# Performance work log

Measured on AMD Instinct MI355X. Metric: run time of the kernel, lower is better.

## Reference

```python
import jax, jax.numpy as jnp
import numpy as np

N_NODES = 100000
N_EDGES = 3200000
D_IN = 128
D_OUT = 128


def setup_inputs() -> dict:
    key = jax.random.key(0)
    k1, k2, k3, k4, k5, k6 = jax.random.split(key, 6)
    inputs = jax.random.normal(k1, (N_NODES, D_IN), dtype=jnp.float32)
    edge_row = jax.random.randint(k2, (N_EDGES,), 0, N_NODES, dtype=jnp.int32)
    edge_col = jax.random.randint(k3, (N_EDGES,), 0, N_NODES, dtype=jnp.int32)
    edge_weight = jax.random.uniform(k4, (N_EDGES,), dtype=jnp.float32)
    # xavier_uniform for [D_IN, D_OUT]
    limit = float(np.sqrt(6.0 / (D_IN + D_OUT)))
    weight = jax.random.uniform(k5, (D_IN, D_OUT), minval=-limit, maxval=limit, dtype=jnp.float32)
    bias = jnp.zeros((D_OUT,), dtype=jnp.float32)
    return {"inputs": inputs, "edge_row": edge_row, "edge_col": edge_col,
            "edge_weight": edge_weight, "weight": weight, "bias": bias}


def reference(inputs, edge_row, edge_col, edge_weight, weight, bias):
    # support = X @ W  -> [N, D_OUT]
    support = inputs @ weight
    # SpMM: out[i] = sum_{e: row[e]==i} w[e] * support[col[e]]
    messages = edge_weight[:, None] * support[edge_col]  # [E, D_OUT]
    out = jax.ops.segment_sum(messages, edge_row, num_segments=N_NODES)
    return out + bias
```

## Files before the change

kernel.cpp:

```cpp
#include <hip/hip_runtime.h>
#include <hip/hip_bf16.h>

#define D 128
#define BROWS 128
#define BSHIFT 7
#define BIN_CHUNK 16384
#define BCAP 5888
#define SORT_CAP 5120

typedef __attribute__((ext_vector_type(8))) short short8;
typedef __attribute__((ext_vector_type(4))) float f32x4;

static __device__ inline unsigned short f2bf(float x) {
    unsigned int u = __float_as_uint(x);
    return (unsigned short)((u + 0x7FFFu + ((u >> 16) & 1u)) >> 16);
}
static __device__ inline float bf2f(unsigned int h16) {
    return __uint_as_float(h16 << 16);
}

__global__ __launch_bounds__(256) void gemm_mfma_kernel(const float* __restrict__ X,
                                                        const float* __restrict__ W,
                                                        unsigned short* __restrict__ Sb,
                                                        int n_rows) {
    __shared__ unsigned char smem[49152];

    const int tid  = threadIdx.x;
    const int row0 = blockIdx.x * 64;

    #pragma unroll
    for (int i = 0; i < 8; ++i) {
        int idx = tid + i * 256;
        int r = idx >> 5, c4 = idx & 31;
        float4 v = make_float4(0.f, 0.f, 0.f, 0.f);
        if (row0 + r < n_rows) v = ((const float4*)(X + (size_t)(row0 + r) * D))[c4];
        uint2 pk;
        pk.x = (unsigned)f2bf(v.x) | ((unsigned)f2bf(v.y) << 16);
        pk.y = (unsigned)f2bf(v.z) | ((unsigned)f2bf(v.w) << 16);
        *(uint2*)(smem + r * 256 + ((c4 * 8) ^ ((r & 7) << 4))) = pk;
    }
    #pragma unroll
    for (int i = 0; i < 8; ++i) {
        int id = tid + i * 256;
        int n = id & 127, kc = id >> 7;
        float f0 = W[(size_t)(kc * 8 + 0) * D + n];
        float f1 = W[(size_t)(kc * 8 + 1) * D + n];
        float f2 = W[(size_t)(kc * 8 + 2) * D + n];
        float f3 = W[(size_t)(kc * 8 + 3) * D + n];
        float f4 = W[(size_t)(kc * 8 + 4) * D + n];
        float f5 = W[(size_t)(kc * 8 + 5) * D + n];
        float f6 = W[(size_t)(kc * 8 + 6) * D + n];
        float f7 = W[(size_t)(kc * 8 + 7) * D + n];
        unsigned pk0 = (unsigned)f2bf(f0) | ((unsigned)f2bf(f1) << 16);
        unsigned pk1 = (unsigned)f2bf(f2) | ((unsigned)f2bf(f3) << 16);
        unsigned pk2 = (unsigned)f2bf(f4) | ((unsigned)f2bf(f5) << 16);
        unsigned pk3 = (unsigned)f2bf(f6) | ((unsigned)f2bf(f7) << 16);
        *(uint4*)(smem + 16384 + n * 256 + ((kc * 16) ^ ((n & 7) << 4))) =
            make_uint4(pk0, pk1, pk2, pk3);
    }
    __syncthreads();

    const int wv  = __builtin_amdgcn_readfirstlane(tid >> 6);
    const int l15 = tid & 15;
    const int lhi = (tid & 63) >> 4;

    f32x4 acc[4][2];
    #pragma unroll
    for (int m = 0; m < 4; ++m)
        #pragma unroll
        for (int j = 0; j < 2; ++j) acc[m][j] = (f32x4){0.f, 0.f, 0.f, 0.f};

    #pragma unroll
    for (int ks = 0; ks < 4; ++ks) {
        const int kb = ks * 64 + lhi * 16;
        short8 a[4], b[2];
        #pragma unroll
        for (int m = 0; m < 4; ++m) {
            int r = m * 16 + l15;
            a[m] = *(const short8*)(smem + r * 256 + (kb ^ ((r & 7) << 4)));
        }
        #pragma unroll
        for (int j = 0; j < 2; ++j) {
            int n = wv * 32 + j * 16 + l15;
            b[j] = *(const short8*)(smem + 16384 + n * 256 + (kb ^ ((n & 7) << 4)));
        }
        #pragma unroll
        for (int m = 0; m < 4; ++m)
            #pragma unroll
            for (int j = 0; j < 2; ++j)
                acc[m][j] = __builtin_amdgcn_mfma_f32_16x16x32_bf16(a[m], b[j],
                                                                   acc[m][j], 0, 0, 0);
    }
    __syncthreads();

    #pragma unroll
    for (int m = 0; m < 4; ++m)
        #pragma unroll
        for (int j = 0; j < 2; ++j)
            #pragma unroll
            for (int r = 0; r < 4; ++r) {
                int row = m * 16 + lhi * 4 + r;
                int col = wv * 32 + j * 16 + l15;
                *(unsigned short*)(smem + row * 256 + ((col * 2) ^ ((row & 7) << 4))) =
                    f2bf(acc[m][j][r]);
            }
    __syncthreads();
    #pragma unroll
    for (int i = 0; i < 4; ++i) {
        int idx = tid + i * 256;
        int r = idx >> 4, kb = (idx & 15) * 16;
        uint4 v = *(const uint4*)(smem + r * 256 + (kb ^ ((r & 7) << 4)));
        int row = row0 + r;
        if (row < n_rows)
            *(uint4*)((unsigned char*)Sb + (size_t)row * 256 + kb) = v;
    }
}

__global__ __launch_bounds__(1024) void binit_kernel(int* __restrict__ curm, int nb) {
    int b = threadIdx.x;
    if (b < nb) curm[b] = b * BCAP;
}

__global__ __launch_bounds__(512) void bin_kernel(const int* __restrict__ erow,
                                                  const int* __restrict__ ecol,
                                                  const float* __restrict__ ew,
                                                  int* __restrict__ curm,
                                                  int2* __restrict__ binned,
                                                  int n_edges, int nb) {
    __shared__ int h[1024];
    __shared__ int base[1024];
    const int c0  = blockIdx.x * BIN_CHUNK;
    const int tid = threadIdx.x;
    int rows[BIN_CHUNK / 512];

    for (int i = tid; i < nb; i += 512) h[i] = 0;
    __syncthreads();
    #pragma unroll
    for (int k = 0; k < BIN_CHUNK / 512; ++k) {
        int e = c0 + k * 512 + tid;
        int r = (e < n_edges) ? erow[e] : -1;
        rows[k] = r;
        if (r >= 0) atomicAdd(&h[r >> BSHIFT], 1);
    }
    __syncthreads();
    for (int b = tid; b < nb; b += 512) {
        int c = h[b];
        if (c) base[b] = atomicAdd(&curm[b], c);
        h[b] = 0;
    }
    __syncthreads();
    #pragma unroll
    for (int k = 0; k < BIN_CHUNK / 512; ++k) {
        int r = rows[k];
        if (r >= 0) {
            int e = c0 + k * 512 + tid;
            int b = r >> BSHIFT;
            int pos = base[b] + atomicAdd(&h[b], 1);
            if (pos < (b + 1) * BCAP) {
                int2 p;
                p.x = (int)(((unsigned)(r & (BROWS - 1)) << 25) | (unsigned)ecol[e]);
                p.y = __float_as_int(ew[e]);
                binned[pos] = p;
            }
        }
    }
}

__global__ __launch_bounds__(512) void csr_sort_kernel(const int* __restrict__ curm,
                                                       int2* __restrict__ binned,
                                                       int2* __restrict__ aux,
                                                       int* __restrict__ offs,
                                                       int* __restrict__ ends,
                                                       int n_nodes) {
    __shared__ int  lhist[BROWS];
    __shared__ int  lscan[BROWS];
    __shared__ int  lcur[BROWS];
    __shared__ int2 staged[SORT_CAP];
    __shared__ unsigned short perm[SORT_CAP];

    const int b    = blockIdx.x;
    const int bs   = b * BCAP;
    const int cb   = min(curm[b] - bs, BCAP);
    const int row0 = b * BROWS;
    const int tid  = threadIdx.x;

    if (tid < BROWS) lhist[tid] = 0;
    __syncthreads();

    if (cb <= SORT_CAP) {
        for (int i = tid; i < cb; i += 512) {
            int2 p = binned[bs + i];
            staged[i] = p;
            atomicAdd(&lhist[(unsigned)p.x >> 25], 1);
        }
        __syncthreads();
        if (tid < BROWS) lscan[tid] = lhist[tid];
        __syncthreads();
        for (int d = 1; d < BROWS; d <<= 1) {
            int t = 0;
            if (tid < BROWS && tid >= d) t = lscan[tid - d];
            __syncthreads();
            if (tid < BROWS) lscan[tid] += t;
            __syncthreads();
        }
        if (tid < BROWS) {
            int excl = lscan[tid] - lhist[tid];
            lcur[tid] = excl;
            if (row0 + tid < n_nodes) {
                offs[row0 + tid] = bs + excl;
                ends[row0 + tid] = bs + lscan[tid];
            }
        }
        __syncthreads();
        for (int i = tid; i < cb; i += 512) {
            int pos = atomicAdd(&lcur[(unsigned)staged[i].x >> 25], 1);
            perm[pos] = (unsigned short)i;
        }
        __syncthreads();
        for (int i = tid; i < cb; i += 512) {
            int2 p = staged[perm[i]];
            binned[bs + i] = make_int2(p.x & 0x1FFFFFF, p.y);
        }
    } else {
        for (int i = tid; i < cb; i += 512)
            atomicAdd(&lhist[(unsigned)binned[bs + i].x >> 25], 1);
        __syncthreads();
        if (tid < BROWS) lscan[tid] = lhist[tid];
        __syncthreads();
        for (int d = 1; d < BROWS; d <<= 1) {
            int t = 0;
            if (tid < BROWS && tid >= d) t = lscan[tid - d];
            __syncthreads();
            if (tid < BROWS) lscan[tid] += t;
            __syncthreads();
        }
        if (tid < BROWS) {
            int excl = lscan[tid] - lhist[tid];
            lcur[tid] = excl;
            if (row0 + tid < n_nodes) {
                offs[row0 + tid] = bs + excl;
                ends[row0 + tid] = bs + lscan[tid];
            }
        }
        __syncthreads();
        for (int i = tid; i < cb; i += 512) aux[bs + i] = binned[bs + i];
        __syncthreads();
        for (int i = tid; i < cb; i += 512) {
            int2 p = aux[bs + i];
            int pos = atomicAdd(&lcur[(unsigned)p.x >> 25], 1);
            binned[bs + pos] = make_int2(p.x & 0x1FFFFFF, p.y);
        }
    }
}

__global__ __launch_bounds__(256) void spmm_csr_kernel(const unsigned short* __restrict__ Sb,
                                                       const int* __restrict__ offs,
                                                       const int* __restrict__ ends,
                                                       const int2* __restrict__ edges,
                                                       const float* __restrict__ bias,
                                                       float* __restrict__ out,
                                                       int n_nodes) {
    const int wv   = __builtin_amdgcn_readfirstlane(threadIdx.x >> 6);
    const int node = blockIdx.x * 4 + wv;
    const int lane = threadIdx.x & 63;
    if (node >= n_nodes) return;
    const int start = offs[node];
    const int end   = ends[node];

    const unsigned* Su = (const unsigned*)Sb;
    float2 b2 = ((const float2*)bias)[lane];
    float ax = b2.x, ay = b2.y;

    int e = start;
    for (; e + 7 < end; e += 8) {
        int2 p[8];
        #pragma unroll
        for (int j = 0; j < 8; ++j) p[j] = edges[e + j];
        unsigned sv[8];
        #pragma unroll
        for (int j = 0; j < 8; ++j) sv[j] = Su[(size_t)p[j].x * 64 + lane];
        #pragma unroll
        for (int j = 0; j < 8; ++j) {
            float w = __int_as_float(p[j].y);
            ax += w * bf2f(sv[j] & 0xFFFFu);
            ay += w * bf2f(sv[j] >> 16);
        }
    }
    for (; e < end; ++e) {
        int2 p = edges[e];
        unsigned s = Su[(size_t)p.x * 64 + lane];
        float w = __int_as_float(p.y);
        ax += w * bf2f(s & 0xFFFFu);
        ay += w * bf2f(s >> 16);
    }

    float2 o; o.x = ax; o.y = ay;
    ((float2*)(out + (size_t)node * D))[lane] = o;
}

__global__ __launch_bounds__(256) void gemm_f32_kernel(const float* __restrict__ X,
                                                       const float* __restrict__ W,
                                                       float* __restrict__ S,
                                                       int n_rows) {
    __shared__ float Ws[D * D];
    __shared__ float Xs[64 * 132];
    const int tid  = threadIdx.x;
    const int row0 = blockIdx.x * 64;
    #pragma unroll
    for (int i = 0; i < 16; ++i) {
        int idx = tid + i * 256;
        ((float4*)Ws)[idx] = ((const float4*)W)[idx];
    }
    #pragma unroll
    for (int i = 0; i < 8; ++i) {
        int idx = tid + i * 256;
        int r = idx >> 5, c4 = idx & 31;
        if (row0 + r < n_rows) {
            float4 v = ((const float4*)(X + (size_t)(row0 + r) * D))[c4];
            *((float4*)&Xs[r * 132 + c4 * 4]) = v;
        }
    }
    __syncthreads();
    const int cg = tid & 15, rg = tid >> 4;
    const int r0 = rg * 4, c0 = cg * 4, c1 = 64 + cg * 4;
    float acc[4][8];
    #pragma unroll
    for (int r = 0; r < 4; ++r)
        #pragma unroll
        for (int c = 0; c < 8; ++c) acc[r][c] = 0.f;
    #pragma unroll 4
    for (int k = 0; k < D; ++k) {
        float4 w0 = *((const float4*)&Ws[k * D + c0]);
        float4 w1 = *((const float4*)&Ws[k * D + c1]);
        #pragma unroll
        for (int r = 0; r < 4; ++r) {
            float x = Xs[(r0 + r) * 132 + k];
            acc[r][0] += x * w0.x; acc[r][1] += x * w0.y;
            acc[r][2] += x * w0.z; acc[r][3] += x * w0.w;
            acc[r][4] += x * w1.x; acc[r][5] += x * w1.y;
            acc[r][6] += x * w1.z; acc[r][7] += x * w1.w;
        }
    }
    #pragma unroll
    for (int r = 0; r < 4; ++r) {
        int row = row0 + r0 + r;
        if (row < n_rows) {
            float4 o0 = {acc[r][0], acc[r][1], acc[r][2], acc[r][3]};
            float4 o1 = {acc[r][4], acc[r][5], acc[r][6], acc[r][7]};
            ((float4*)(S + (size_t)row * D))[cg]      = o0;
            ((float4*)(S + (size_t)row * D))[16 + cg] = o1;
        }
    }
}

__global__ __launch_bounds__(256) void init_out_kernel(float* __restrict__ out,
                                                       const float* __restrict__ bias,
                                                       int total4) {
    int idx = blockIdx.x * blockDim.x + threadIdx.x;
    int stride = gridDim.x * blockDim.x;
    for (; idx < total4; idx += stride) {
        float4 b = ((const float4*)bias)[idx & 31];
        ((float4*)out)[idx] = b;
    }
}

__global__ __launch_bounds__(256) void spmm_atomic_kernel(const float* __restrict__ S,
                                                          const int* __restrict__ erow,
                                                          const int* __restrict__ ecol,
                                                          const float* __restrict__ ew,
                                                          float* __restrict__ out,
                                                          int n_edges) {
    const int lane   = threadIdx.x & 63;
    const int wave   = blockIdx.x * (blockDim.x >> 6) + (threadIdx.x >> 6);
    const int nwaves = gridDim.x * (blockDim.x >> 6);
    for (int e = wave; e < n_edges; e += nwaves) {
        int   col = ecol[e];
        int   row = erow[e];
        float w   = ew[e];
        float2 s  = *(((const float2*)(S + (size_t)col * D)) + lane);
        float* op = out + (size_t)row * D + lane * 2;
        unsafeAtomicAdd(op,     w * s.x);
        unsafeAtomicAdd(op + 1, w * s.y);
    }
}

extern "C" void kernel_launch(void* const* d_in, const int* in_sizes, int n_in,
                              void* d_out, int out_size, void* d_ws, size_t ws_size,
                              hipStream_t stream) {
    const float* X    = (const float*)d_in[0];
    const int*   erow = (const int*)  d_in[1];
    const int*   ecol = (const int*)  d_in[2];
    const float* ew   = (const float*)d_in[3];
    const float* W    = (const float*)d_in[4];
    const float* bias = (const float*)d_in[5];
    float* out = (float*)d_out;

    const int n_nodes = in_sizes[0] / D;
    const int n_edges = in_sizes[1];
    const int nb      = (n_nodes + BROWS - 1) / BROWS;

    size_t sb_bytes   = (size_t)n_nodes * D * sizeof(unsigned short);
    size_t curm_bytes = ((size_t)nb * sizeof(int) + 15) & ~(size_t)15;
    size_t offs_bytes = ((size_t)n_nodes * sizeof(int) + 15) & ~(size_t)15;
    size_t bin_bytes  = (size_t)nb * BCAP * sizeof(int2);
    size_t need = sb_bytes + curm_bytes + 2 * offs_bytes + bin_bytes + 64;
    bool aux_ok = (size_t)out_size * sizeof(float) >= bin_bytes;

    if (ws_size >= need && nb <= 1024 && aux_ok) {
        char* p = (char*)d_ws;
        unsigned short* Sb = (unsigned short*)p;  p += sb_bytes;
        int* curm = (int*)p;                      p += curm_bytes;
        int* offs = (int*)p;                      p += offs_bytes;
        int* ends = (int*)p;                      p += offs_bytes;
        p = (char*)(((uintptr_t)p + 15) & ~(uintptr_t)15);
        int2* binned = (int2*)p;

        gemm_mfma_kernel<<<(n_nodes + 63) / 64, 256, 0, stream>>>(X, W, Sb, n_nodes);
        binit_kernel<<<1, 1024, 0, stream>>>(curm, nb);
        bin_kernel<<<(n_edges + BIN_CHUNK - 1) / BIN_CHUNK, 512, 0, stream>>>(
            erow, ecol, ew, curm, binned, n_edges, nb);
        csr_sort_kernel<<<nb, 512, 0, stream>>>(curm, binned, (int2*)out,
                                                offs, ends, n_nodes);
        spmm_csr_kernel<<<(n_nodes + 3) / 4, 256, 0, stream>>>(Sb, offs, ends, binned,
                                                               bias, out, n_nodes);
    } else {
        float* S = (float*)d_ws;
        gemm_f32_kernel<<<(n_nodes + 63) / 64, 256, 0, stream>>>(X, W, S, n_nodes);
        init_out_kernel<<<2048, 256, 0, stream>>>(out, bias, n_nodes * (D / 4));
        spmm_atomic_kernel<<<2048, 256, 0, stream>>>(S, erow, ecol, ew, out, n_edges);
    }
}
```

Measured before the change: 185.0 us.

## Fuse bin init into GEMM, enlarge GEMM tiles, vectorize edge loads in binning

New measurement: 176.9 us. -4.4%, faster.

```diff
diff --git a/kernel.cpp b/kernel.cpp
--- a/kernel.cpp
+++ b/kernel.cpp
@@ -19,18 +19,23 @@
     return __uint_as_float(h16 << 16);
 }
 
-__global__ __launch_bounds__(256) void gemm_mfma_kernel(const float* __restrict__ X,
+__global__ __launch_bounds__(512) void gemm_mfma_kernel(const float* __restrict__ X,
                                                         const float* __restrict__ W,
                                                         unsigned short* __restrict__ Sb,
-                                                        int n_rows) {
-    __shared__ unsigned char smem[49152];
+                                                        int n_rows,
+                                                        int* __restrict__ curm, int nb) {
+    __shared__ unsigned char smem[65536];
 
     const int tid  = threadIdx.x;
-    const int row0 = blockIdx.x * 64;
+    const int row0 = blockIdx.x * 128;
+
+    if (blockIdx.x == 0 && curm) {
+        for (int b = tid; b < nb; b += 512) curm[b] = b * BCAP;
+    }
 
     #pragma unroll
     for (int i = 0; i < 8; ++i) {
-        int idx = tid + i * 256;
+        int idx = tid + i * 512;
         int r = idx >> 5, c4 = idx & 31;
         float4 v = make_float4(0.f, 0.f, 0.f, 0.f);
         if (row0 + r < n_rows) v = ((const float4*)(X + (size_t)(row0 + r) * D))[c4];
@@ -40,8 +45,8 @@
         *(uint2*)(smem + r * 256 + ((c4 * 8) ^ ((r & 7) << 4))) = pk;
     }
     #pragma unroll
-    for (int i = 0; i < 8; ++i) {
-        int id = tid + i * 256;
+    for (int i = 0; i < 4; ++i) {
+        int id = tid + i * 512;
         int n = id & 127, kc = id >> 7;
         float f0 = W[(size_t)(kc * 8 + 0) * D + n];
         float f1 = W[(size_t)(kc * 8 + 1) * D + n];
@@ -55,7 +60,7 @@
         unsigned pk1 = (unsigned)f2bf(f2) | ((unsigned)f2bf(f3) << 16);
         unsigned pk2 = (unsigned)f2bf(f4) | ((unsigned)f2bf(f5) << 16);
         unsigned pk3 = (unsigned)f2bf(f6) | ((unsigned)f2bf(f7) << 16);
-        *(uint4*)(smem + 16384 + n * 256 + ((kc * 16) ^ ((n & 7) << 4))) =
+        *(uint4*)(smem + 32768 + n * 256 + ((kc * 16) ^ ((n & 7) << 4))) =
             make_uint4(pk0, pk1, pk2, pk3);
     }
     __syncthreads();
@@ -64,61 +69,49 @@
     const int l15 = tid & 15;
     const int lhi = (tid & 63) >> 4;
 
-    f32x4 acc[4][2];
-    #pragma unroll
-    for (int m = 0; m < 4; ++m)
-        #pragma unroll
-        for (int j = 0; j < 2; ++j) acc[m][j] = (f32x4){0.f, 0.f, 0.f, 0.f};
+    f32x4 acc[8];
+    #pragma unroll
+    for (int m = 0; m < 8; ++m) acc[m] = (f32x4){0.f, 0.f, 0.f, 0.f};
 
     #pragma unroll
     for (int ks = 0; ks < 4; ++ks) {
         const int kb = ks * 64 + lhi * 16;
-        short8 a[4], b[2];
-        #pragma unroll
-        for (int m = 0; m < 4; ++m) {
+        short8 b;
+        {
+            int n = wv * 16 + l15;
+            b = *(const short8*)(smem + 32768 + n * 256 + (kb ^ ((n & 7) << 4)));
+        }
+        short8 a[8];
+        #pragma unroll
+        for (int m = 0; m < 8; ++m) {
             int r = m * 16 + l15;
             a[m] = *(const short8*)(smem + r * 256 + (kb ^ ((r & 7) << 4)));
         }
         #pragma unroll
-        for (int j = 0; j < 2; ++j) {
-            int n = wv * 32 + j * 16 + l15;
-            b[j] = *(const short8*)(smem + 16384 + n * 256 + (kb ^ ((n & 7) << 4)));
-        }
-        #pragma unroll
-        for (int m = 0; m < 4; ++m)
-            #pragma unroll
-            for (int j = 0; j < 2; ++j)
-                acc[m][j] = __builtin_amdgcn_mfma_f32_16x16x32_bf16(a[m], b[j],
-                                                                   acc[m][j], 0, 0, 0);
-    }
-    __syncthreads();
-
-    #pragma unroll
-    for (int m = 0; m < 4; ++m)
-        #pragma unroll
-        for (int j = 0; j < 2; ++j)
-            #pragma unroll
-            for (int r = 0; r < 4; ++r) {
-                int row = m * 16 + lhi * 4 + r;
-                int col = wv * 32 + j * 16 + l15;
-                *(unsigned short*)(smem + row * 256 + ((col * 2) ^ ((row & 7) << 4))) =
-                    f2bf(acc[m][j][r]);
-            }
+        for (int m = 0; m < 8; ++m)
+            acc[m] = __builtin_amdgcn_mfma_f32_16x16x32_bf16(a[m], b, acc[m], 0, 0, 0);
+    }
+    __syncthreads();
+
+    #pragma unroll
+    for (int m = 0; m < 8; ++m)
+        #pragma unroll
+        for (int r = 0; r < 4; ++r) {
+            int row = m * 16 + lhi * 4 + r;
+            int col = wv * 16 + l15;
+            *(unsigned short*)(smem + row * 256 + ((col * 2) ^ ((row & 7) << 4))) =
+                f2bf(acc[m][r]);
+        }
     __syncthreads();
     #pragma unroll
     for (int i = 0; i < 4; ++i) {
-        int idx = tid + i * 256;
+        int idx = tid + i * 512;
         int r = idx >> 4, kb = (idx & 15) * 16;
         uint4 v = *(const uint4*)(smem + r * 256 + (kb ^ ((r & 7) << 4)));
         int row = row0 + r;
         if (row < n_rows)
             *(uint4*)((unsigned char*)Sb + (size_t)row * 256 + kb) = v;
     }
-}
-
-__global__ __launch_bounds__(1024) void binit_kernel(int* __restrict__ curm, int nb) {
-    int b = threadIdx.x;
-    if (b < nb) curm[b] = b * BCAP;
 }
 
 __global__ __launch_bounds__(512) void bin_kernel(const int* __restrict__ erow,
@@ -131,16 +124,28 @@
     __shared__ int base[1024];
     const int c0  = blockIdx.x * BIN_CHUNK;
     const int tid = threadIdx.x;
-    int rows[BIN_CHUNK / 512];
+    int rows[32];
 
     for (int i = tid; i < nb; i += 512) h[i] = 0;
     __syncthreads();
     #pragma unroll
-    for (int k = 0; k < BIN_CHUNK / 512; ++k) {
-        int e = c0 + k * 512 + tid;
-        int r = (e < n_edges) ? erow[e] : -1;
-        rows[k] = r;
-        if (r >= 0) atomicAdd(&h[r >> BSHIFT], 1);
+    for (int k = 0; k < 8; ++k) {
+        int e = c0 + (k * 512 + tid) * 4;
+        int4 r4;
+        if (e + 3 < n_edges) {
+            r4 = ((const int4*)erow)[e >> 2];
+        } else {
+            r4.x = (e     < n_edges) ? erow[e]     : -1;
+            r4.y = (e + 1 < n_edges) ? erow[e + 1] : -1;
+            r4.z = (e + 2 < n_edges) ? erow[e + 2] : -1;
+            r4.w = (e + 3 < n_edges) ? erow[e + 3] : -1;
+        }
+        rows[k * 4 + 0] = r4.x; rows[k * 4 + 1] = r4.y;
+        rows[k * 4 + 2] = r4.z; rows[k * 4 + 3] = r4.w;
+        if (r4.x >= 0) atomicAdd(&h[r4.x >> BSHIFT], 1);
+        if (r4.y >= 0) atomicAdd(&h[r4.y >> BSHIFT], 1);
+        if (r4.z >= 0) atomicAdd(&h[r4.z >> BSHIFT], 1);
+        if (r4.w >= 0) atomicAdd(&h[r4.w >> BSHIFT], 1);
     }
     __syncthreads();
     for (int b = tid; b < nb; b += 512) {
@@ -150,17 +155,36 @@
     }
     __syncthreads();
     #pragma unroll
-    for (int k = 0; k < BIN_CHUNK / 512; ++k) {
-        int r = rows[k];
-        if (r >= 0) {
-            int e = c0 + k * 512 + tid;
-            int b = r >> BSHIFT;
-            int pos = base[b] + atomicAdd(&h[b], 1);
-            if (pos < (b + 1) * BCAP) {
-                int2 p;
-                p.x = (int)(((unsigned)(r & (BROWS - 1)) << 25) | (unsigned)ecol[e]);
-                p.y = __float_as_int(ew[e]);
-                binned[pos] = p;
+    for (int k = 0; k < 8; ++k) {
+        int e = c0 + (k * 512 + tid) * 4;
+        int4   cv; float4 wv;
+        if (e + 3 < n_edges) {
+            cv = ((const int4*)ecol)[e >> 2];
+            wv = ((const float4*)ew)[e >> 2];
+        } else {
+            cv.x = (e     < n_edges) ? ecol[e]     : 0;
+            cv.y = (e + 1 < n_edges) ? ecol[e + 1] : 0;
+            cv.z = (e + 2 < n_edges) ? ecol[e + 2] : 0;
+            cv.w = (e + 3 < n_edges) ? ecol[e + 3] : 0;
+            wv.x = (e     < n_edges) ? ew[e]     : 0.f;
+            wv.y = (e + 1 < n_edges) ? ew[e + 1] : 0.f;
+            wv.z = (e + 2 < n_edges) ? ew[e + 2] : 0.f;
+            wv.w = (e + 3 < n_edges) ? ew[e + 3] : 0.f;
+        }
+        int   cs[4] = {cv.x, cv.y, cv.z, cv.w};
+        float ws[4] = {wv.x, wv.y, wv.z, wv.w};
+        #pragma unroll
+        for (int j = 0; j < 4; ++j) {
+            int r = rows[k * 4 + j];
+            if (r >= 0) {
+                int b = r >> BSHIFT;
+                int pos = base[b] + atomicAdd(&h[b], 1);
+                if (pos < (b + 1) * BCAP) {
+                    int2 p;
+                    p.x = (int)(((unsigned)(r & (BROWS - 1)) << 25) | (unsigned)cs[j]);
+                    p.y = __float_as_int(ws[j]);
+                    binned[pos] = p;
+                }
             }
         }
     }
@@ -415,8 +439,8 @@
         p = (char*)(((uintptr_t)p + 15) & ~(uintptr_t)15);
         int2* binned = (int2*)p;
 
-        gemm_mfma_kernel<<<(n_nodes + 63) / 64, 256, 0, stream>>>(X, W, Sb, n_nodes);
-        binit_kernel<<<1, 1024, 0, stream>>>(curm, nb);
+        gemm_mfma_kernel<<<(n_nodes + 127) / 128, 512, 0, stream>>>(
+            X, W, Sb, n_nodes, curm, nb);
         bin_kernel<<<(n_edges + BIN_CHUNK - 1) / BIN_CHUNK, 512, 0, stream>>>(
             erow, ecol, ew, curm, binned, n_edges, nb);
         csr_sort_kernel<<<nb, 512, 0, stream>>>(curm, binned, (int2*)out,
```
